# Kernel optimization log

Hardware: AMD Instinct MI355X
Metric: run time of the kernel (lower is better)

The kernel has to match this reference:

```python
import jax, jax.numpy as jnp
import numpy as np
from jax import lax

B, L = 4, 1024
D_MODEL, D_INNER, D_STATE, D_CONV, DT_RANK, N_LAYERS = 256, 512, 16, 4, 16, 4
BN_EPS = 1e-5


def setup_inputs() -> dict:
    key = jax.random.key(0)
    ks = jax.random.split(key, 16)
    nrm = lambda k, s, sc: jax.random.normal(k, s, jnp.float32) * sc
    inp = {
        "x": nrm(ks[0], (B, L), 1.0),
        "y": nrm(ks[1], (B, L), 1.0),  # accepted but unused by forward
        # embedding: Conv1d(1 -> D_MODEL, k=3, same, no bias) + BatchNorm1d (inference stats) + SiLU
        "emb_w": nrm(ks[2], (D_MODEL, 1, 3), 1.0 / np.sqrt(3.0)),
        "bn_gamma": 1.0 + nrm(ks[3], (D_MODEL,), 0.1),
        "bn_beta": nrm(ks[4], (D_MODEL,), 0.1),
        "bn_mean": nrm(ks[5], (D_MODEL,), 0.1),
        "bn_var": jax.random.uniform(ks[6], (D_MODEL,), jnp.float32, 0.5, 1.5),
        # stacked Mamba layer params (leading dim = layer)
        "in_proj_w": nrm(ks[7], (N_LAYERS, 2 * D_INNER, D_MODEL), 1.0 / np.sqrt(D_MODEL)),
        "conv_w": nrm(ks[8], (N_LAYERS, D_INNER, 1, D_CONV), 1.0 / np.sqrt(D_CONV)),
        "conv_b": nrm(ks[9], (N_LAYERS, D_INNER), 0.02),
        "x_proj_w": nrm(ks[10], (N_LAYERS, DT_RANK + 2 * D_STATE, D_INNER), 1.0 / np.sqrt(D_INNER)),
        "dt_proj_w": nrm(ks[11], (N_LAYERS, D_INNER, DT_RANK), 1.0 / np.sqrt(DT_RANK)),
        # inverse-softplus of dt in [1e-3, 0.1] (mamba init)
        "dt_proj_b": jnp.log(jnp.expm1(jax.random.uniform(ks[12], (N_LAYERS, D_INNER), jnp.float32, 1e-3, 0.1))),
        # S4D-real init: A = -[1..N]
        "A_log": jnp.log(jnp.tile(jnp.arange(1, D_STATE + 1, dtype=jnp.float32)[None, None, :], (N_LAYERS, D_INNER, 1))),
        "D_skip": jnp.ones((N_LAYERS, D_INNER), jnp.float32),
        "out_proj_w": nrm(ks[13], (N_LAYERS, D_MODEL, D_INNER), 1.0 / np.sqrt(D_INNER)),
    }
    return inp


def selective_scan(u, dt, A, Bc, Cc, D_skip):
    # u, dt: (B,L,Di); A: (Di,N); Bc, Cc: (B,L,N)
    dA = jnp.exp(dt[..., None] * A)                              # (B,L,Di,N)
    dBu = dt[..., None] * Bc[:, :, None, :] * u[..., None]       # (B,L,Di,N)

    def step(h, xs):
        dA_t, dBu_t, C_t = xs
        h = dA_t * h + dBu_t                                      # (B,Di,N)
        y_t = jnp.einsum('bdn,bn->bd', h, C_t)
        return h, y_t

    h0 = jnp.zeros((u.shape[0], u.shape[2], A.shape[1]), u.dtype)
    _, ys = lax.scan(step, h0, (dA.swapaxes(0, 1), dBu.swapaxes(0, 1), Cc.swapaxes(0, 1)))
    return ys.swapaxes(0, 1) + u * D_skip                         # (B,L,Di)


def mamba_block(h, in_w, cw, cb, xp_w, dtp_w, dtp_b, A_log, D_skip, out_w):
    xz = jnp.einsum('bld,ed->ble', h, in_w)                       # (B,L,2Di)
    xi, z = jnp.split(xz, 2, axis=-1)
    # causal depthwise conv1d over time
    xc = lax.conv_general_dilated(xi.swapaxes(1, 2), cw, (1,), [(D_CONV - 1, 0)],
                                  dimension_numbers=('NCH', 'OIH', 'NCH'),
                                  feature_group_count=D_INNER) + cb[None, :, None]
    xc = jax.nn.silu(xc).swapaxes(1, 2)                           # (B,L,Di)
    xdbl = jnp.einsum('bld,ed->ble', xc, xp_w)                    # (B,L,dt_rank+2N)
    dt, Bc, Cc = jnp.split(xdbl, [DT_RANK, DT_RANK + D_STATE], axis=-1)
    dt = jax.nn.softplus(jnp.einsum('blr,dr->bld', dt, dtp_w) + dtp_b)
    A = -jnp.exp(A_log)                                           # (Di,N)
    y = selective_scan(xc, dt, A, Bc, Cc, D_skip)
    y = y * jax.nn.silu(z)
    return jnp.einsum('bld,od->blo', y, out_w)                    # (B,L,D_MODEL)


def reference(x, y, emb_w, bn_gamma, bn_beta, bn_mean, bn_var, in_proj_w, conv_w,
              conv_b, x_proj_w, dt_proj_w, dt_proj_b, A_log, D_skip, out_proj_w):
    h = x[:, None, :]                                             # (B,1,L)
    h = lax.conv_general_dilated(h, emb_w, (1,), 'SAME', dimension_numbers=('NCH', 'OIH', 'NCH'))
    inv = lax.rsqrt(bn_var + BN_EPS)
    h = (h - bn_mean[None, :, None]) * (inv * bn_gamma)[None, :, None] + bn_beta[None, :, None]
    h = jax.nn.silu(h).swapaxes(1, 2)                             # (B,L,D_MODEL)
    for i in range(N_LAYERS):
        h = mamba_block(h, in_proj_w[i], conv_w[i], conv_b[i], x_proj_w[i],
                        dt_proj_w[i], dt_proj_b[i], A_log[i], D_skip[i], out_proj_w[i])
    return h.sum(axis=-1)                                         # (B,L)
```

## Files before the change

### kernel.cpp

```cpp
#include <hip/hip_runtime.h>
#include <math.h>

#define BATCH 4
#define SEQL 1024
#define DMODEL 256
#define DINNER 512
#define DSTATE 16
#define DTRANK 16
#define NLAYERS 4
#define MTOT (BATCH * SEQL)

#define IDX(t) ((((t) & 63) * 17) + ((t) >> 6))

static __device__ __forceinline__ float siluf(float x) {
    return x / (1.0f + __expf(-x));
}
static __device__ __forceinline__ float softplusf(float x) {
    return (x > 0.0f) ? (x + __logf(1.0f + __expf(-x))) : __logf(1.0f + __expf(x));
}

__global__ void k_embed(const float* __restrict__ x, const float* __restrict__ emb_w,
                        const float* __restrict__ gamma, const float* __restrict__ beta,
                        const float* __restrict__ mean, const float* __restrict__ var,
                        float* __restrict__ h) {
    const int m = blockIdx.x;
    const int d = threadIdx.x;
    const int b = m >> 10;
    const int l = m & 1023;
    const float xm1 = (l > 0)    ? x[b * SEQL + l - 1] : 0.0f;
    const float x0  =              x[b * SEQL + l];
    const float xp1 = (l < 1023) ? x[b * SEQL + l + 1] : 0.0f;
    float c = xm1 * emb_w[d * 3 + 0] + x0 * emb_w[d * 3 + 1] + xp1 * emb_w[d * 3 + 2];
    const float inv = 1.0f / sqrtf(var[d] + 1e-5f);
    c = (c - mean[d]) * (inv * gamma[d]) + beta[d];
    h[(size_t)m * DMODEL + d] = siluf(c);
}

template <int BM, int BN, int BK, int TM, int TN, bool AKM, int KTOT, int KSPLIT>
__global__ __launch_bounds__((BM / TM) * (BN / TN))
void sgemm2(const float* __restrict__ A, int lda,
            const float* __restrict__ Bw, int ldb,
            float* __restrict__ C, int ldc, int mstride) {
    constexpr int TX = BN / TN;
    constexpr int TY = BM / TM;
    constexpr int NT = TX * TY;
    static_assert(NT == 256, "expect 256 threads");
    constexpr int KS = KTOT / KSPLIT;
    static_assert(KS % BK == 0, "");
    constexpr int NSTEPS = KS / BK;
    constexpr int A4 = BM * BK / 4;
    constexpr int B4 = BN * BK / 4;
    constexpr int APT = (A4 + NT - 1) / NT;
    constexpr int BPT = (B4 + NT - 1) / NT;
    constexpr bool AG = (A4 % NT) != 0;
    constexpr bool BG = (B4 % NT) != 0;

    const int tid = threadIdx.x;
    const int tx = tid % TX;
    const int ty = tid / TX;
    const int m0 = blockIdx.y * BM;
    const int n0 = blockIdx.x * BN;
    const int kt0 = blockIdx.z * KS;

    __shared__ float As[BK][BM + 4];
    __shared__ float Bs[BK][BN + 4];

    float acc[TM][TN] = {};
    float4 ra[APT], rb[BPT];

    auto loadA = [&](int kt) {
#pragma unroll
        for (int u = 0; u < APT; ++u) {
            const int v = tid + u * NT;
            if (!AG || v < A4) {
                if (AKM) {
                    const int kk = v / (BM / 4);
                    const int i4 = v % (BM / 4);
                    ra[u] = *reinterpret_cast<const float4*>(
                        &A[(size_t)(kt + kk) * lda + m0 + i4 * 4]);
                } else {
                    const int i = v / (BK / 4);
                    const int jv = v % (BK / 4);
                    ra[u] = *reinterpret_cast<const float4*>(
                        &A[(size_t)(m0 + i) * lda + kt + jv * 4]);
                }
            }
        }
    };
    auto loadB = [&](int kt) {
#pragma unroll
        for (int u = 0; u < BPT; ++u) {
            const int v = tid + u * NT;
            if (!BG || v < B4) {
                const int i = v / (BK / 4);
                const int jv = v % (BK / 4);
                rb[u] = *reinterpret_cast<const float4*>(
                    &Bw[(size_t)(n0 + i) * ldb + kt + jv * 4]);
            }
        }
    };
    auto storeAB = [&]() {
#pragma unroll
        for (int u = 0; u < APT; ++u) {
            const int v = tid + u * NT;
            if (!AG || v < A4) {
                if (AKM) {
                    const int kk = v / (BM / 4);
                    const int i4 = v % (BM / 4);
                    *reinterpret_cast<float4*>(&As[kk][i4 * 4]) = ra[u];
                } else {
                    const int i = v / (BK / 4);
                    const int jv = v % (BK / 4);
                    As[jv * 4 + 0][i] = ra[u].x;
                    As[jv * 4 + 1][i] = ra[u].y;
                    As[jv * 4 + 2][i] = ra[u].z;
                    As[jv * 4 + 3][i] = ra[u].w;
                }
            }
        }
#pragma unroll
        for (int u = 0; u < BPT; ++u) {
            const int v = tid + u * NT;
            if (!BG || v < B4) {
                const int i = v / (BK / 4);
                const int jv = v % (BK / 4);
                Bs[jv * 4 + 0][i] = rb[u].x;
                Bs[jv * 4 + 1][i] = rb[u].y;
                Bs[jv * 4 + 2][i] = rb[u].z;
                Bs[jv * 4 + 3][i] = rb[u].w;
            }
        }
    };

    loadA(kt0);
    loadB(kt0);

    for (int s = 0; s < NSTEPS; ++s) {
        storeAB();
        __syncthreads();
        if (s + 1 < NSTEPS) {
            loadA(kt0 + (s + 1) * BK);
            loadB(kt0 + (s + 1) * BK);
        }
#pragma unroll
        for (int k = 0; k < BK; ++k) {
            float a[TM], b[TN];
#pragma unroll
            for (int i = 0; i < TM; ++i) a[i] = As[k][ty * TM + i];
#pragma unroll
            for (int j = 0; j < TN; ++j) b[j] = Bs[k][tx * TN + j];
#pragma unroll
            for (int i = 0; i < TM; ++i)
#pragma unroll
                for (int j = 0; j < TN; ++j) acc[i][j] = fmaf(a[i], b[j], acc[i][j]);
        }
        __syncthreads();
    }

    float* Cz = C + (size_t)blockIdx.z * mstride;
#pragma unroll
    for (int i = 0; i < TM; ++i) {
        const int m = m0 + ty * TM + i;
#pragma unroll
        for (int j = 0; j < TN; ++j) {
            const int n = n0 + tx * TN + j;
            Cz[(size_t)m * ldc + n] = acc[i][j];
        }
    }
}

template <int KS>
__global__ __launch_bounds__(512) void k_kred(const float* __restrict__ part,
                                              float* __restrict__ out, int n4) {
    const int i = blockIdx.x * 512 + threadIdx.x;
    if (i >= n4) return;
    const float4* p = reinterpret_cast<const float4*>(part);
    float4 s = p[i];
#pragma unroll
    for (int z = 1; z < KS; ++z) {
        const float4 t = p[i + (size_t)z * n4];
        s.x += t.x; s.y += t.y; s.z += t.z; s.w += t.w;
    }
    reinterpret_cast<float4*>(out)[i] = s;
}

__global__ __launch_bounds__(256) void k_convT(const float* __restrict__ xzT,
                                               const float* __restrict__ cw,
                                               const float* __restrict__ cb,
                                               float* __restrict__ xcT) {
    const int d = blockIdx.x;
    const int b = blockIdx.y;
    const float w0 = cw[d * 4 + 0], w1 = cw[d * 4 + 1];
    const float w2 = cw[d * 4 + 2], w3 = cw[d * 4 + 3];
    const float bias = cb[d];
    const float* row = xzT + (size_t)d * MTOT + b * SEQL;
    float* orow = xcT + (size_t)d * MTOT + b * SEQL;
    for (int t = threadIdx.x; t < SEQL; t += 256) {
        float acc = fmaf(row[t], w3, bias);
        if (t >= 1) acc = fmaf(row[t - 1], w2, acc);
        if (t >= 2) acc = fmaf(row[t - 2], w1, acc);
        if (t >= 3) acc = fmaf(row[t - 3], w0, acc);
        orow[t] = siluf(acc);
    }
}

#define CCH 64
#define CT 16

__global__ __launch_bounds__(1024) void k_scan6(
    const float* __restrict__ xcT, const float* __restrict__ xdbl,
    const float* __restrict__ xzT, const float* __restrict__ dtw,
    const float* __restrict__ dtb, const float* __restrict__ A_log,
    const float* __restrict__ D_skip, float* __restrict__ yT) {
    const int d = blockIdx.x;
    const int b = blockIdx.y;
    const int tid = threadIdx.x;
    const int c = tid >> 4;
    const int n = tid & 15;

    __shared__ float dt_s[1088];
    __shared__ float u_s[1088];
    __shared__ float p_s[1088];
    __shared__ float PS[CCH][17][2];

    const int mbase = b * SEQL;

    const float4 w0 = *reinterpret_cast<const float4*>(&dtw[d * 16 + 0]);
    const float4 w1 = *reinterpret_cast<const float4*>(&dtw[d * 16 + 4]);
    const float4 w2 = *reinterpret_cast<const float4*>(&dtw[d * 16 + 8]);
    const float4 w3 = *reinterpret_cast<const float4*>(&dtw[d * 16 + 12]);
    const float bias = dtb[d];

    {
        const int t = tid;
        const float* xr = &xdbl[(size_t)(mbase + t) * 48];
        const float4 a0 = *reinterpret_cast<const float4*>(&xr[0]);
        const float4 a1 = *reinterpret_cast<const float4*>(&xr[4]);
        const float4 a2 = *reinterpret_cast<const float4*>(&xr[8]);
        const float4 a3 = *reinterpret_cast<const float4*>(&xr[12]);
        float s = bias;
        s = fmaf(a0.x, w0.x, s); s = fmaf(a0.y, w0.y, s);
        s = fmaf(a0.z, w0.z, s); s = fmaf(a0.w, w0.w, s);
        s = fmaf(a1.x, w1.x, s); s = fmaf(a1.y, w1.y, s);
        s = fmaf(a1.z, w1.z, s); s = fmaf(a1.w, w1.w, s);
        s = fmaf(a2.x, w2.x, s); s = fmaf(a2.y, w2.y, s);
        s = fmaf(a2.z, w2.z, s); s = fmaf(a2.w, w2.w, s);
        s = fmaf(a3.x, w3.x, s); s = fmaf(a3.y, w3.y, s);
        s = fmaf(a3.z, w3.z, s); s = fmaf(a3.w, w3.w, s);
        dt_s[IDX(t)] = softplusf(s);
        u_s[IDX(t)]  = xcT[(size_t)d * MTOT + mbase + t];
    }
    __syncthreads();

    const float a = -__expf(A_log[d * DSTATE + n]);
    const int t0 = c * CT;
    const int loc_base = (c & 3) * 272 + (c >> 2);

    const float* Bp = &xdbl[(size_t)(mbase + t0) * 48 + DTRANK + n];
    const float* Cp = Bp + DSTATE;

    float P = 1.0f, S = 0.0f;
#pragma unroll
    for (int j = 0; j < CT; ++j) {
        const float Bv = Bp[j * 48];
        const int loc = j * 17 + loc_base;
        const float dtv = dt_s[loc];
        const float ee = __expf(dtv * a);
        P *= ee;
        S = fmaf(ee, S, dtv * Bv * u_s[loc]);
    }
    PS[c][n][0] = P;
    PS[c][n][1] = S;
    __syncthreads();

    float h = 0.0f;
    for (int j = 0; j < c; ++j) h = fmaf(PS[j][n][0], h, PS[j][n][1]);

#pragma unroll
    for (int j = 0; j < CT; ++j) {
        const float Bv = Bp[j * 48];
        const float Cv = Cp[j * 48];
        const int loc = j * 17 + loc_base;
        const float dtv = dt_s[loc];
        const float ee = __expf(dtv * a);
        h = fmaf(ee, h, dtv * Bv * u_s[loc]);
        float p = h * Cv;
        p += __shfl_xor(p, 1);
        p += __shfl_xor(p, 2);
        p += __shfl_xor(p, 4);
        p += __shfl_xor(p, 8);
        if (n == 0) p_s[j * 17 + loc_base] = p;
    }
    __syncthreads();

    const float Dsk = D_skip[d];
    {
        const int t = tid;
        const float uv = u_s[IDX(t)];
        const float zv = xzT[(size_t)(DINNER + d) * MTOT + mbase + t];
        yT[(size_t)d * MTOT + mbase + t] = (p_s[IDX(t)] + uv * Dsk) * siluf(zv);
    }
}

__global__ void k_wsum(const float* __restrict__ w, float* __restrict__ wsum) {
    const int d = threadIdx.x;
    float s = 0.0f;
    for (int o = 0; o < DMODEL; ++o) s += w[(size_t)o * DINNER + d];
    wsum[d] = s;
}

__global__ __launch_bounds__(256) void k_finalT(const float* __restrict__ yT,
                                                const float* __restrict__ wsum,
                                                float* __restrict__ out) {
    const int tid = threadIdx.x;
    const int dg = tid >> 5;
    const int ml = tid & 31;
    const int m = blockIdx.x * 32 + ml;
    float acc = 0.0f;
    const int dbase = dg * 64;
#pragma unroll 8
    for (int dd = 0; dd < 64; ++dd)
        acc = fmaf(yT[(size_t)(dbase + dd) * MTOT + m], wsum[dbase + dd], acc);
    __shared__ float red[8][33];
    red[dg][ml] = acc;
    __syncthreads();
    if (dg == 0) {
        float s = 0.0f;
#pragma unroll
        for (int g = 0; g < 8; ++g) s += red[g][ml];
        out[m] = s;
    }
}

extern "C" void kernel_launch(void* const* d_in, const int* in_sizes, int n_in,
                              void* d_out, int out_size, void* d_ws, size_t ws_size,
                              hipStream_t stream) {
    const float* x        = (const float*)d_in[0];
    const float* emb_w    = (const float*)d_in[2];
    const float* bn_gamma = (const float*)d_in[3];
    const float* bn_beta  = (const float*)d_in[4];
    const float* bn_mean  = (const float*)d_in[5];
    const float* bn_var   = (const float*)d_in[6];
    const float* in_proj_w  = (const float*)d_in[7];
    const float* conv_w     = (const float*)d_in[8];
    const float* conv_b     = (const float*)d_in[9];
    const float* x_proj_w   = (const float*)d_in[10];
    const float* dt_proj_w  = (const float*)d_in[11];
    const float* dt_proj_b  = (const float*)d_in[12];
    const float* A_log      = (const float*)d_in[13];
    const float* D_skip     = (const float*)d_in[14];
    const float* out_proj_w = (const float*)d_in[15];
    float* out = (float*)d_out;
    float* ws = (float*)d_ws;

    float* h    = ws;
    float* xzT  = h + (size_t)MTOT * DMODEL;
    float* xcT  = xzT + (size_t)1024 * MTOT;
    float* xdbl = xcT + (size_t)DINNER * MTOT;
    float* yT   = xdbl + (size_t)MTOT * 48;
    float* wsum = yT + (size_t)DINNER * MTOT;
    float* partX = yT;
    float* partO = xzT;

    k_embed<<<MTOT, DMODEL, 0, stream>>>(x, emb_w, bn_gamma, bn_beta, bn_mean, bn_var, h);

    for (int i = 0; i < NLAYERS; ++i) {
        const float* in_w  = in_proj_w + (size_t)i * 2 * DINNER * DMODEL;
        const float* cw    = conv_w + (size_t)i * DINNER * 4;
        const float* cb    = conv_b + (size_t)i * DINNER;
        const float* xp_w  = x_proj_w + (size_t)i * 48 * DINNER;
        const float* dtp_w = dt_proj_w + (size_t)i * DINNER * DTRANK;
        const float* dtp_b = dt_proj_b + (size_t)i * DINNER;
        const float* Al    = A_log + (size_t)i * DINNER * DSTATE;
        const float* Dsk   = D_skip + (size_t)i * DINNER;
        const float* o_w   = out_proj_w + (size_t)i * DMODEL * DINNER;

        sgemm2<64, 128, 16, 4, 8, false, DMODEL, 1>
            <<<dim3(MTOT / 128, 1024 / 64, 1), 256, 0, stream>>>(
                in_w, DMODEL, h, DMODEL, xzT, MTOT, 0);

        k_convT<<<dim3(DINNER, BATCH), 256, 0, stream>>>(xzT, cw, cb, xcT);

        sgemm2<64, 48, 16, 4, 3, true, DINNER, 8>
            <<<dim3(1, MTOT / 64, 8), 256, 0, stream>>>(
                xcT, MTOT, xp_w, DINNER, partX, 48, MTOT * 48);
        k_kred<8><<<(MTOT * 48 / 4 + 511) / 512, 512, 0, stream>>>(
            partX, xdbl, MTOT * 48 / 4);

        k_scan6<<<dim3(DINNER, BATCH), 1024, 0, stream>>>(
            xcT, xdbl, xzT, dtp_w, dtp_b, Al, Dsk, yT);

        if (i < NLAYERS - 1) {
            sgemm2<64, 64, 16, 4, 4, true, DINNER, 2>
                <<<dim3(DMODEL / 64, MTOT / 64, 2), 256, 0, stream>>>(
                    yT, MTOT, o_w, DINNER, partO, DMODEL, MTOT * DMODEL);
            k_kred<2><<<(MTOT * DMODEL / 4 + 511) / 512, 512, 0, stream>>>(
                partO, h, MTOT * DMODEL / 4);
        } else {
            k_wsum<<<1, DINNER, 0, stream>>>(o_w, wsum);
            k_finalT<<<MTOT / 32, 256, 0, stream>>>(yT, wsum, out);
        }
    }
}
```

Before: 507.7 us.

## Give each scan thread four states and shrink scan blocks to 256

The selective-scan kernel now assigns four state dimensions to each thread instead of one and launches 256-thread blocks instead of 1024. B and C are loaded as float4, the chunk carry table is written and read as float4, and the per-timestep reduction needs two shuffles instead of four. Staging and epilogue loops now cover the 1024 timesteps in four passes. This is meant to cut redundant loads of dt and u, shuffle traffic and per-block overhead. The cost is more registers per thread and less thread-level parallelism for hiding latency.

```diff
diff --git a/kernel.cpp b/kernel.cpp
--- a/kernel.cpp
+++ b/kernel.cpp
@@ -207,7 +207,7 @@
 #define CCH 64
 #define CT 16
 
-__global__ __launch_bounds__(1024) void k_scan6(
+__global__ __launch_bounds__(256) void k_scan7(
     const float* __restrict__ xcT, const float* __restrict__ xdbl,
     const float* __restrict__ xzT, const float* __restrict__ dtw,
     const float* __restrict__ dtb, const float* __restrict__ A_log,
@@ -215,13 +215,13 @@
     const int d = blockIdx.x;
     const int b = blockIdx.y;
     const int tid = threadIdx.x;
-    const int c = tid >> 4;
-    const int n = tid & 15;
+    const int c = tid >> 2;
+    const int nq = tid & 3;
 
     __shared__ float dt_s[1088];
     __shared__ float u_s[1088];
     __shared__ float p_s[1088];
-    __shared__ float PS[CCH][17][2];
+    __shared__ float PS[CCH][18][2];
 
     const int mbase = b * SEQL;
 
@@ -231,8 +231,9 @@
     const float4 w3 = *reinterpret_cast<const float4*>(&dtw[d * 16 + 12]);
     const float bias = dtb[d];
 
-    {
-        const int t = tid;
+#pragma unroll
+    for (int ph = 0; ph < 4; ++ph) {
+        const int t = ph * 256 + tid;
         const float* xr = &xdbl[(size_t)(mbase + t) * 48];
         const float4 a0 = *reinterpret_cast<const float4*>(&xr[0]);
         const float4 a1 = *reinterpret_cast<const float4*>(&xr[4]);
@@ -252,50 +253,79 @@
     }
     __syncthreads();
 
-    const float a = -__expf(A_log[d * DSTATE + n]);
+    const float4 al = *reinterpret_cast<const float4*>(&A_log[d * DSTATE + nq * 4]);
+    const float a0 = -__expf(al.x);
+    const float a1 = -__expf(al.y);
+    const float a2 = -__expf(al.z);
+    const float a3 = -__expf(al.w);
+
     const int t0 = c * CT;
     const int loc_base = (c & 3) * 272 + (c >> 2);
 
-    const float* Bp = &xdbl[(size_t)(mbase + t0) * 48 + DTRANK + n];
+    const float* Bp = &xdbl[(size_t)(mbase + t0) * 48 + DTRANK + nq * 4];
     const float* Cp = Bp + DSTATE;
 
-    float P = 1.0f, S = 0.0f;
+    float P0 = 1.0f, P1 = 1.0f, P2 = 1.0f, P3 = 1.0f;
+    float S0 = 0.0f, S1 = 0.0f, S2 = 0.0f, S3 = 0.0f;
 #pragma unroll
     for (int j = 0; j < CT; ++j) {
-        const float Bv = Bp[j * 48];
+        const float4 B4 = *reinterpret_cast<const float4*>(&Bp[j * 48]);
         const int loc = j * 17 + loc_base;
         const float dtv = dt_s[loc];
-        const float ee = __expf(dtv * a);
-        P *= ee;
-        S = fmaf(ee, S, dtv * Bv * u_s[loc]);
-    }
-    PS[c][n][0] = P;
-    PS[c][n][1] = S;
+        const float du = dtv * u_s[loc];
+        const float e0 = __expf(dtv * a0);
+        const float e1 = __expf(dtv * a1);
+        const float e2 = __expf(dtv * a2);
+        const float e3 = __expf(dtv * a3);
+        P0 *= e0; P1 *= e1; P2 *= e2; P3 *= e3;
+        S0 = fmaf(e0, S0, B4.x * du);
+        S1 = fmaf(e1, S1, B4.y * du);
+        S2 = fmaf(e2, S2, B4.z * du);
+        S3 = fmaf(e3, S3, B4.w * du);
+    }
+    {
+        float4* ps0 = reinterpret_cast<float4*>(&PS[c][nq * 4][0]);
+        ps0[0] = make_float4(P0, S0, P1, S1);
+        ps0[1] = make_float4(P2, S2, P3, S3);
+    }
     __syncthreads();
 
-    float h = 0.0f;
-    for (int j = 0; j < c; ++j) h = fmaf(PS[j][n][0], h, PS[j][n][1]);
+    float h0 = 0.0f, h1 = 0.0f, h2 = 0.0f, h3 = 0.0f;
+    for (int j = 0; j < c; ++j) {
+        const float4 q0 = *reinterpret_cast<const float4*>(&PS[j][nq * 4][0]);
+        const float4 q1 = *reinterpret_cast<const float4*>(&PS[j][nq * 4 + 2][0]);
+        h0 = fmaf(q0.x, h0, q0.y);
+        h1 = fmaf(q0.z, h1, q0.w);
+        h2 = fmaf(q1.x, h2, q1.y);
+        h3 = fmaf(q1.z, h3, q1.w);
+    }
 
 #pragma unroll
     for (int j = 0; j < CT; ++j) {
-        const float Bv = Bp[j * 48];
-        const float Cv = Cp[j * 48];
+        const float4 B4 = *reinterpret_cast<const float4*>(&Bp[j * 48]);
+        const float4 C4 = *reinterpret_cast<const float4*>(&Cp[j * 48]);
         const int loc = j * 17 + loc_base;
         const float dtv = dt_s[loc];
-        const float ee = __expf(dtv * a);
-        h = fmaf(ee, h, dtv * Bv * u_s[loc]);
-        float p = h * Cv;
+        const float du = dtv * u_s[loc];
+        const float e0 = __expf(dtv * a0);
+        const float e1 = __expf(dtv * a1);
+        const float e2 = __expf(dtv * a2);
+        const float e3 = __expf(dtv * a3);
+        h0 = fmaf(e0, h0, B4.x * du);
+        h1 = fmaf(e1, h1, B4.y * du);
+        h2 = fmaf(e2, h2, B4.z * du);
+        h3 = fmaf(e3, h3, B4.w * du);
+        float p = fmaf(h0, C4.x, fmaf(h1, C4.y, fmaf(h2, C4.z, h3 * C4.w)));
         p += __shfl_xor(p, 1);
         p += __shfl_xor(p, 2);
-        p += __shfl_xor(p, 4);
-        p += __shfl_xor(p, 8);
-        if (n == 0) p_s[j * 17 + loc_base] = p;
+        if (nq == 0) p_s[loc] = p;
     }
     __syncthreads();
 
     const float Dsk = D_skip[d];
-    {
-        const int t = tid;
+#pragma unroll
+    for (int ph = 0; ph < 4; ++ph) {
+        const int t = ph * 256 + tid;
         const float uv = u_s[IDX(t)];
         const float zv = xzT[(size_t)(DINNER + d) * MTOT + mbase + t];
         yT[(size_t)d * MTOT + mbase + t] = (p_s[IDX(t)] + uv * Dsk) * siluf(zv);
@@ -387,7 +417,7 @@
         k_kred<8><<<(MTOT * 48 / 4 + 511) / 512, 512, 0, stream>>>(
             partX, xdbl, MTOT * 48 / 4);
 
-        k_scan6<<<dim3(DINNER, BATCH), 1024, 0, stream>>>(
+        k_scan7<<<dim3(DINNER, BATCH), 256, 0, stream>>>(
             xcT, xdbl, xzT, dtp_w, dtp_b, Al, Dsk, yT);
 
         if (i < NLAYERS - 1) {
```

New measurement: 446.8 us. 12.0% less time.
